# Performance work log

Hardware: AMD Instinct MI355X
Metric: run time of the kernel (lower is better)

The kernel has to match this reference:

```python
import jax, jax.numpy as jnp
import numpy as np

N_NODES = 10000
N_EDGES = 640000
D_IN = 128
D_OUT = 128


def setup_inputs() -> dict:
    key = jax.random.key(0)
    k_x, k_val, k_w, k_row, k_col = jax.random.split(key, 5)
    # Glorot init for weight, zeros for bias (matches _weight_init)
    limit = float(np.sqrt(6.0 / (D_IN + D_OUT)))
    weight = jax.random.uniform(k_w, (D_IN, D_OUT), jnp.float32, -limit, limit)
    return {
        "x": jax.random.normal(k_x, (N_NODES, D_IN), jnp.float32),
        "adj_val": jax.random.uniform(k_val, (N_EDGES,), jnp.float32),  # normalized edge weights of sparse adj
        "weight": weight,
        "bias": jnp.zeros((D_OUT,), jnp.float32),
        "adj_row": jax.random.randint(k_row, (N_EDGES,), 0, N_NODES, jnp.int32),
        "adj_col": jax.random.randint(k_col, (N_EDGES,), 0, N_NODES, jnp.int32),
    }


def reference(x, adj_val, weight, bias, adj_row, adj_col):
    # dense GEMM: h = x @ W  -> [N, D_OUT]
    h = jnp.matmul(x, weight)
    # SpMM with COO adjacency: out[r] = sum_{e: row[e]=r} val[e] * h[col[e]]
    msg = adj_val[:, None] * h[adj_col]  # [E, D_OUT] gather + scale
    out = jax.ops.segment_sum(msg, adj_row, num_segments=x.shape[0])
    return out + bias
```

## Files before the change

### kernel.cpp

```cpp
#include <hip/hip_runtime.h>

#define N_NODES 10000
#define N_EDGES 640000
#define D 128
#define NQ (N_EDGES / 4)

#define GRID1 512
#define GEMM_BLOCKS 157
#define SCAT_BLOCKS (GRID1 - GEMM_BLOCKS)
#define NBUCK 79
#define BCAP 10240
#define CAP2 128
#define QPAD2 144
#define OVF_CAP 8192
#define LSTR 136

typedef unsigned int uint32;
typedef unsigned long long u64;
typedef unsigned short u16;
using short8 = __attribute__((ext_vector_type(8))) short;
using f32x4  = __attribute__((ext_vector_type(4))) float;

__device__ __forceinline__ uint32 f2bf_bits(float f) {
    uint32 u = __float_as_uint(f);
    return (u + 0x7FFFu + ((u >> 16) & 1u)) >> 16;
}
__device__ __forceinline__ uint32 pack2(float lo, float hi) {
    return f2bf_bits(lo) | (f2bf_bits(hi) << 16);
}

__device__ __forceinline__ void ovf_push(int r, uint32 rc, int* ovf_cnt, u64* ovf) {
    int o = atomicAdd(ovf_cnt, 1);
    if (o < OVF_CAP)
        __hip_atomic_store(&ovf[o], ((u64)(uint32)r << 32) | rc,
                           __ATOMIC_RELAXED, __HIP_MEMORY_SCOPE_AGENT);
}

__global__ __launch_bounds__(256, 4) void gemm_scatter_kernel(
    const float* __restrict__ x, const float* __restrict__ w,
    const int* __restrict__ row, const int* __restrict__ col,
    const float* __restrict__ val,
    uint32* __restrict__ h2, int* __restrict__ gcnt,
    int* __restrict__ ovf_cnt, u64* __restrict__ ovf,
    uint2* __restrict__ bstore)
{
    __shared__ __align__(16) u16 Ws[128 * LSTR];
    const int t = threadIdx.x;
    const int lane = t & 63;
    const int wid  = t >> 6;

    if (blockIdx.x < GEMM_BLOCKS) {
        const int q = lane >> 4, cl = lane & 15;

        #pragma unroll
        for (int i = 0; i < 32; ++i) {
            int lin = t + i * 256;
            int c = lin & 127;
            int m = lin >> 7;
            float w0 = w[(2 * m) * D + c];
            float w1 = w[(2 * m + 1) * D + c];
            *(uint32*)&Ws[c * LSTR + 2 * m] = pack2(w0, w1);
        }

        int gr = blockIdx.x * 64 + wid * 16 + cl;
        if (gr >= N_NODES) gr = N_NODES - 1;
        const float* xrow = &x[(size_t)gr * D];
        float4 xv[8];
        #pragma unroll
        for (int kk = 0; kk < 4; ++kk) {
            xv[2 * kk]     = *(const float4*)&xrow[kk * 32 + q * 8];
            xv[2 * kk + 1] = *(const float4*)&xrow[kk * 32 + q * 8 + 4];
        }
        __syncthreads();

        f32x4 acc[8] = {};
        #pragma unroll
        for (int kk = 0; kk < 4; ++kk) {
            union { short8 s; uint32 u[4]; } af;
            float4 a = xv[2 * kk], b = xv[2 * kk + 1];
            af.u[0] = pack2(a.x, a.y); af.u[1] = pack2(a.z, a.w);
            af.u[2] = pack2(b.x, b.y); af.u[3] = pack2(b.z, b.w);
            #pragma unroll
            for (int ct = 0; ct < 8; ++ct) {
                short8 bf = *(const short8*)&Ws[(ct * 16 + cl) * LSTR + kk * 32 + q * 8];
                acc[ct] = __builtin_amdgcn_mfma_f32_16x16x32_bf16(af.s, bf, acc[ct], 0, 0, 0);
            }
        }
        #pragma unroll
        for (int reg = 0; reg < 4; ++reg) {
            int node = blockIdx.x * 64 + wid * 16 + q * 4 + reg;
            if (node < N_NODES) {
                uint32* base = h2 + (size_t)node * 64 + cl;
                #pragma unroll
                for (int ct = 0; ct < 4; ++ct)
                    base[ct * 16] = pack2(acc[ct][reg], acc[ct + 4][reg]);
            }
        }
    } else {
        int* lcnt  = (int*)Ws;
        int* lbase = (int*)Ws + 96;
        int* lcnt2 = (int*)Ws + 192;
        if (t < NBUCK) lcnt[t] = 0;
        __syncthreads();

        const int sb = blockIdx.x - GEMM_BLOCKS;
        const int4*   row4 = (const int4*)row;
        const int4*   col4 = (const int4*)col;
        const float4* val4 = (const float4*)val;

        for (int i = sb * 256 + t; i < NQ; i += SCAT_BLOCKS * 256) {
            int4 r = row4[i];
            atomicAdd(&lcnt[r.x >> 7], 1);
            atomicAdd(&lcnt[r.y >> 7], 1);
            atomicAdd(&lcnt[r.z >> 7], 1);
            atomicAdd(&lcnt[r.w >> 7], 1);
        }
        __syncthreads();
        if (t < NBUCK) {
            int c = lcnt[t];
            lbase[t] = (c > 0) ? atomicAdd(&gcnt[t], c) : 0;
            lcnt2[t] = 0;
        }
        __syncthreads();

        for (int i = sb * 256 + t; i < NQ; i += SCAT_BLOCKS * 256) {
            int4 r = row4[i]; int4 c = col4[i]; float4 v = val4[i];
            #pragma unroll
            for (int e = 0; e < 4; ++e) {
                int rr = (e == 0) ? r.x : (e == 1) ? r.y : (e == 2) ? r.z : r.w;
                int cc = (e == 0) ? c.x : (e == 1) ? c.y : (e == 2) ? c.z : c.w;
                float vv = (e == 0) ? v.x : (e == 1) ? v.y : (e == 2) ? v.z : v.w;
                uint32 rc = (uint32)cc | (f2bf_bits(vv) << 16);
                int b = rr >> 7;
                int k = atomicAdd(&lcnt2[b], 1);
                int pos = lbase[b] + k;
                if (pos < BCAP)
                    bstore[(size_t)b * BCAP + pos] = make_uint2(rc, (uint32)rr);
                else
                    ovf_push(rr, rc, ovf_cnt, ovf);
            }
        }
    }
}

__global__ __launch_bounds__(256) void spmm_kernel(
    const uint2* __restrict__ bstore, const int* __restrict__ gcnt,
    int* __restrict__ ovf_cnt, u64* __restrict__ ovf,
    const uint32* __restrict__ h2, const float* __restrict__ bias,
    float* __restrict__ out)
{
    __shared__ uint32 qbuf[4 * QPAD2];
    __shared__ int cnt[4];
    const int t = threadIdx.x;
    const int lane = t & 63;
    const int wid  = t >> 6;
    const int r0 = blockIdx.x * 4;
    const int b  = r0 >> 7;

    if (t < 4) cnt[t] = 0;
    __syncthreads();

    int n = gcnt[b]; if (n > BCAP) n = BCAP;
    for (int i = t; i < n; i += 256) {
        uint2 e = bstore[(size_t)b * BCAP + i];
        uint32 d = e.y - (uint32)r0;
        if (d < 4u) {
            int k = atomicAdd(&cnt[d], 1);
            if (k < CAP2) qbuf[d * QPAD2 + k] = e.x;
            else ovf_push((int)e.y, e.x, ovf_cnt, ovf);
        }
    }
    __syncthreads();

    const int r = r0 + wid;
    uint32* qb = &qbuf[wid * QPAD2];
    int ntot = cnt[wid]; if (ntot > CAP2) ntot = CAP2;
    if (lane < 16) qb[ntot + lane] = 0;
    __builtin_amdgcn_s_waitcnt(0);

    const int npad = (ntot + 7) & ~7;
    float a0 = 0.f, a1 = 0.f;

    uint32 rq0,rq1,rq2,rq3,rq4,rq5,rq6,rq7;
    uint32 hh0,hh1,hh2,hh3,hh4,hh5,hh6,hh7;
    rq0 = qb[0]; hh0 = h2[((rq0 & 0xFFFFu) << 6) + lane];
    rq1 = qb[1]; hh1 = h2[((rq1 & 0xFFFFu) << 6) + lane];
    rq2 = qb[2]; hh2 = h2[((rq2 & 0xFFFFu) << 6) + lane];
    rq3 = qb[3]; hh3 = h2[((rq3 & 0xFFFFu) << 6) + lane];
    rq4 = qb[4]; hh4 = h2[((rq4 & 0xFFFFu) << 6) + lane];
    rq5 = qb[5]; hh5 = h2[((rq5 & 0xFFFFu) << 6) + lane];
    rq6 = qb[6]; hh6 = h2[((rq6 & 0xFFFFu) << 6) + lane];
    rq7 = qb[7]; hh7 = h2[((rq7 & 0xFFFFu) << 6) + lane];

#define CONSUME_PREFETCH(RQ, HH, P)                                          \
    {                                                                        \
        a0 = fmaf(__uint_as_float(RQ & 0xFFFF0000u),                         \
                  __uint_as_float(HH << 16), a0);                            \
        a1 = fmaf(__uint_as_float(RQ & 0xFFFF0000u),                         \
                  __uint_as_float(HH & 0xFFFF0000u), a1);                    \
        uint32 rn = qb[j + 8 + P];                                           \
        RQ = rn; HH = h2[((rn & 0xFFFFu) << 6) + lane];                      \
    }

    for (int j = 0; j < npad; j += 8) {
        CONSUME_PREFETCH(rq0, hh0, 0)
        CONSUME_PREFETCH(rq1, hh1, 1)
        CONSUME_PREFETCH(rq2, hh2, 2)
        CONSUME_PREFETCH(rq3, hh3, 3)
        CONSUME_PREFETCH(rq4, hh4, 4)
        CONSUME_PREFETCH(rq5, hh5, 5)
        CONSUME_PREFETCH(rq6, hh6, 6)
        CONSUME_PREFETCH(rq7, hh7, 7)
    }
#undef CONSUME_PREFETCH

    int novf = __hip_atomic_load(ovf_cnt, __ATOMIC_RELAXED, __HIP_MEMORY_SCOPE_AGENT);
    if (novf > OVF_CAP) novf = OVF_CAP;
    for (int k = 0; k < novf; ++k) {
        u64 e = __hip_atomic_load(&ovf[k], __ATOMIC_RELAXED, __HIP_MEMORY_SCOPE_AGENT);
        if ((uint32)(e >> 32) == (uint32)r) {
            uint32 qq = (uint32)e;
            uint32 hv = h2[((qq & 0xFFFFu) << 6) + lane];
            a0 = fmaf(__uint_as_float(qq & 0xFFFF0000u), __uint_as_float(hv << 16), a0);
            a1 = fmaf(__uint_as_float(qq & 0xFFFF0000u), __uint_as_float(hv & 0xFFFF0000u), a1);
        }
    }

    out[(size_t)r * D + lane]      = a0 + bias[lane];
    out[(size_t)r * D + 64 + lane] = a1 + bias[lane + 64];
}

extern "C" void kernel_launch(void* const* d_in, const int* in_sizes, int n_in,
                              void* d_out, int out_size, void* d_ws, size_t ws_size,
                              hipStream_t stream)
{
    const float* x    = (const float*)d_in[0];
    const float* aval = (const float*)d_in[1];
    const float* w    = (const float*)d_in[2];
    const float* bias = (const float*)d_in[3];
    const int* arow   = (const int*)d_in[4];
    const int* acol   = (const int*)d_in[5];

    char* ws = (char*)d_ws;
    uint32* h2     = (uint32*)(ws);
    int*    gcnt   = (int*)(ws + 2560000);
    int*    ovfcnt = (int*)(ws + 2560320);
    u64*    ovf    = (u64*)(ws + 2560384);
    uint2*  bstore = (uint2*)(ws + 2625920);

    hipMemsetAsync(ws + 2560000, 0, 324, stream);

    gemm_scatter_kernel<<<GRID1, 256, 0, stream>>>(
        x, w, arow, acol, aval, h2, gcnt, ovfcnt, ovf, bstore);
    spmm_kernel<<<N_NODES / 4, 256, 0, stream>>>(
        bstore, gcnt, ovfcnt, ovf, h2, bias, (float*)d_out);
}
```

Before: 121.7 us.

## Replace global-atomic bucket scatter with per-chunk fixed slots and drop memset

The edge scatter now gives each of 256 chunk blocks a fixed slot region per row bucket, using only LDS atomics and a single pass, so it no longer needs a count pass or global atomics. Overflow goes to per-chunk spill arrays, and the memset launch is removed because every count is written unconditionally. The SpMM kernel handles 8 rows per block and scans all 256×96 slots of a bucket, which are padded and mostly empty. The W load is also vectorized to float4. The cost is that the consumer reads more sparsely populated slots and every thread checks the spill counts.

```diff
diff --git a/kernel.cpp b/kernel.cpp
--- a/kernel.cpp
+++ b/kernel.cpp
@@ -5,18 +5,19 @@
 #define D 128
 #define NQ (N_EDGES / 4)
 
-#define GRID1 512
+#define NCHUNK 256
+#define QPC (NQ / NCHUNK)
 #define GEMM_BLOCKS 157
-#define SCAT_BLOCKS (GRID1 - GEMM_BLOCKS)
+#define GRID1 (NCHUNK + GEMM_BLOCKS)
 #define NBUCK 79
-#define BCAP 10240
+#define CCAP 96
+#define SLOTS (NCHUNK * CCAP)
+#define SPILLCAP 2500
 #define CAP2 128
 #define QPAD2 144
-#define OVF_CAP 8192
 #define LSTR 136
 
 typedef unsigned int uint32;
-typedef unsigned long long u64;
 typedef unsigned short u16;
 using short8 = __attribute__((ext_vector_type(8))) short;
 using f32x4  = __attribute__((ext_vector_type(4))) float;
@@ -27,42 +28,76 @@
 }
 __device__ __forceinline__ uint32 pack2(float lo, float hi) {
     return f2bf_bits(lo) | (f2bf_bits(hi) << 16);
-}
-
-__device__ __forceinline__ void ovf_push(int r, uint32 rc, int* ovf_cnt, u64* ovf) {
-    int o = atomicAdd(ovf_cnt, 1);
-    if (o < OVF_CAP)
-        __hip_atomic_store(&ovf[o], ((u64)(uint32)r << 32) | rc,
-                           __ATOMIC_RELAXED, __HIP_MEMORY_SCOPE_AGENT);
 }
 
 __global__ __launch_bounds__(256, 4) void gemm_scatter_kernel(
     const float* __restrict__ x, const float* __restrict__ w,
     const int* __restrict__ row, const int* __restrict__ col,
     const float* __restrict__ val,
-    uint32* __restrict__ h2, int* __restrict__ gcnt,
-    int* __restrict__ ovf_cnt, u64* __restrict__ ovf,
-    uint2* __restrict__ bstore)
+    uint32* __restrict__ h2, int* __restrict__ cnts,
+    int* __restrict__ spillcnt, uint2* __restrict__ bstore,
+    uint2* __restrict__ spill)
 {
     __shared__ __align__(16) u16 Ws[128 * LSTR];
     const int t = threadIdx.x;
-    const int lane = t & 63;
-    const int wid  = t >> 6;
-
-    if (blockIdx.x < GEMM_BLOCKS) {
+
+    if (blockIdx.x < NCHUNK) {
+        int* lcnt = (int*)Ws;
+        if (t < 96) lcnt[t] = 0;
+        __syncthreads();
+
+        const int sb = blockIdx.x;
+        const int4*   row4 = (const int4*)row;
+        const int4*   col4 = (const int4*)col;
+        const float4* val4 = (const float4*)val;
+        const int i0 = sb * QPC;
+        for (int i = i0 + t; i < i0 + QPC; i += 256) {
+            int4 r = row4[i]; int4 c = col4[i]; float4 v = val4[i];
+            #pragma unroll
+            for (int e = 0; e < 4; ++e) {
+                int rr = (e == 0) ? r.x : (e == 1) ? r.y : (e == 2) ? r.z : r.w;
+                int cc = (e == 0) ? c.x : (e == 1) ? c.y : (e == 2) ? c.z : c.w;
+                float vv = (e == 0) ? v.x : (e == 1) ? v.y : (e == 2) ? v.z : v.w;
+                uint32 rc = (uint32)cc | (f2bf_bits(vv) << 16);
+                int b = rr >> 7;
+                int k = atomicAdd(&lcnt[b], 1);
+                if (k < CCAP)
+                    bstore[(size_t)(b * NCHUNK + sb) * CCAP + k] =
+                        make_uint2(rc, (uint32)rr);
+                else {
+                    int ks = atomicAdd(&lcnt[95], 1);
+                    spill[(size_t)sb * SPILLCAP + ks] = make_uint2(rc, (uint32)rr);
+                }
+            }
+        }
+        __syncthreads();
+        if (t < NBUCK) {
+            int c = lcnt[t];
+            cnts[t * NCHUNK + sb] = (c < CCAP) ? c : CCAP;
+        }
+        if (t == 96) spillcnt[sb] = lcnt[95];
+    } else {
+        const int g = blockIdx.x - NCHUNK;
+        const int lane = t & 63;
+        const int wid  = t >> 6;
         const int q = lane >> 4, cl = lane & 15;
 
-        #pragma unroll
-        for (int i = 0; i < 32; ++i) {
+        const float4* w4 = (const float4*)w;
+        #pragma unroll
+        for (int i = 0; i < 8; ++i) {
             int lin = t + i * 256;
-            int c = lin & 127;
-            int m = lin >> 7;
-            float w0 = w[(2 * m) * D + c];
-            float w1 = w[(2 * m + 1) * D + c];
-            *(uint32*)&Ws[c * LSTR + 2 * m] = pack2(w0, w1);
-        }
-
-        int gr = blockIdx.x * 64 + wid * 16 + cl;
+            int m  = lin >> 5;
+            int qc = lin & 31;
+            float4 r0 = w4[(2 * m) * 32 + qc];
+            float4 r1 = w4[(2 * m + 1) * 32 + qc];
+            int c = qc * 4;
+            *(uint32*)&Ws[(c + 0) * LSTR + 2 * m] = pack2(r0.x, r1.x);
+            *(uint32*)&Ws[(c + 1) * LSTR + 2 * m] = pack2(r0.y, r1.y);
+            *(uint32*)&Ws[(c + 2) * LSTR + 2 * m] = pack2(r0.z, r1.z);
+            *(uint32*)&Ws[(c + 3) * LSTR + 2 * m] = pack2(r0.w, r1.w);
+        }
+
+        int gr = g * 64 + wid * 16 + cl;
         if (gr >= N_NODES) gr = N_NODES - 1;
         const float* xrow = &x[(size_t)gr * D];
         float4 xv[8];
@@ -88,7 +123,7 @@
         }
         #pragma unroll
         for (int reg = 0; reg < 4; ++reg) {
-            int node = blockIdx.x * 64 + wid * 16 + q * 4 + reg;
+            int node = g * 64 + wid * 16 + q * 4 + reg;
             if (node < N_NODES) {
                 uint32* base = h2 + (size_t)node * 64 + cl;
                 #pragma unroll
@@ -96,101 +131,75 @@
                     base[ct * 16] = pack2(acc[ct][reg], acc[ct + 4][reg]);
             }
         }
-    } else {
-        int* lcnt  = (int*)Ws;
-        int* lbase = (int*)Ws + 96;
-        int* lcnt2 = (int*)Ws + 192;
-        if (t < NBUCK) lcnt[t] = 0;
-        __syncthreads();
-
-        const int sb = blockIdx.x - GEMM_BLOCKS;
-        const int4*   row4 = (const int4*)row;
-        const int4*   col4 = (const int4*)col;
-        const float4* val4 = (const float4*)val;
-
-        for (int i = sb * 256 + t; i < NQ; i += SCAT_BLOCKS * 256) {
-            int4 r = row4[i];
-            atomicAdd(&lcnt[r.x >> 7], 1);
-            atomicAdd(&lcnt[r.y >> 7], 1);
-            atomicAdd(&lcnt[r.z >> 7], 1);
-            atomicAdd(&lcnt[r.w >> 7], 1);
-        }
-        __syncthreads();
-        if (t < NBUCK) {
-            int c = lcnt[t];
-            lbase[t] = (c > 0) ? atomicAdd(&gcnt[t], c) : 0;
-            lcnt2[t] = 0;
-        }
-        __syncthreads();
-
-        for (int i = sb * 256 + t; i < NQ; i += SCAT_BLOCKS * 256) {
-            int4 r = row4[i]; int4 c = col4[i]; float4 v = val4[i];
-            #pragma unroll
-            for (int e = 0; e < 4; ++e) {
-                int rr = (e == 0) ? r.x : (e == 1) ? r.y : (e == 2) ? r.z : r.w;
-                int cc = (e == 0) ? c.x : (e == 1) ? c.y : (e == 2) ? c.z : c.w;
-                float vv = (e == 0) ? v.x : (e == 1) ? v.y : (e == 2) ? v.z : v.w;
-                uint32 rc = (uint32)cc | (f2bf_bits(vv) << 16);
-                int b = rr >> 7;
-                int k = atomicAdd(&lcnt2[b], 1);
-                int pos = lbase[b] + k;
-                if (pos < BCAP)
-                    bstore[(size_t)b * BCAP + pos] = make_uint2(rc, (uint32)rr);
-                else
-                    ovf_push(rr, rc, ovf_cnt, ovf);
-            }
-        }
     }
 }
 
 __global__ __launch_bounds__(256) void spmm_kernel(
-    const uint2* __restrict__ bstore, const int* __restrict__ gcnt,
-    int* __restrict__ ovf_cnt, u64* __restrict__ ovf,
+    const uint2* __restrict__ bstore, const int* __restrict__ cnts,
+    const int* __restrict__ spillcnt, const uint2* __restrict__ spill,
     const uint32* __restrict__ h2, const float* __restrict__ bias,
     float* __restrict__ out)
 {
-    __shared__ uint32 qbuf[4 * QPAD2];
-    __shared__ int cnt[4];
+    __shared__ uint32 qbuf[8 * QPAD2];
+    __shared__ int lcnts[NCHUNK];
+    __shared__ int cnt[8];
     const int t = threadIdx.x;
     const int lane = t & 63;
     const int wid  = t >> 6;
-    const int r0 = blockIdx.x * 4;
+    const int r0 = blockIdx.x * 8;
     const int b  = r0 >> 7;
 
-    if (t < 4) cnt[t] = 0;
+    lcnts[t] = cnts[b * NCHUNK + t];
+    if (t < 8) cnt[t] = 0;
     __syncthreads();
 
-    int n = gcnt[b]; if (n > BCAP) n = BCAP;
-    for (int i = t; i < n; i += 256) {
-        uint2 e = bstore[(size_t)b * BCAP + i];
-        uint32 d = e.y - (uint32)r0;
-        if (d < 4u) {
-            int k = atomicAdd(&cnt[d], 1);
-            if (k < CAP2) qbuf[d * QPAD2 + k] = e.x;
-            else ovf_push((int)e.y, e.x, ovf_cnt, ovf);
+    for (int i = t; i < SLOTS; i += 256) {
+        int ch = i / CCAP;
+        int sl = i - ch * CCAP;
+        if (sl < lcnts[ch]) {
+            uint2 e = bstore[(size_t)b * SLOTS + i];
+            uint32 d = e.y - (uint32)r0;
+            if (d < 8u) {
+                int k = atomicAdd(&cnt[d], 1);
+                if (k < CAP2) qbuf[d * QPAD2 + k] = e.x;
+            }
+        }
+    }
+    {
+        int sc = spillcnt[t];
+        for (int k = 0; k < sc; ++k) {
+            uint2 e = spill[(size_t)t * SPILLCAP + k];
+            uint32 d = e.y - (uint32)r0;
+            if (d < 8u) {
+                int k2 = atomicAdd(&cnt[d], 1);
+                if (k2 < CAP2) qbuf[d * QPAD2 + k2] = e.x;
+            }
         }
     }
     __syncthreads();
 
-    const int r = r0 + wid;
-    uint32* qb = &qbuf[wid * QPAD2];
-    int ntot = cnt[wid]; if (ntot > CAP2) ntot = CAP2;
-    if (lane < 16) qb[ntot + lane] = 0;
-    __builtin_amdgcn_s_waitcnt(0);
-
-    const int npad = (ntot + 7) & ~7;
-    float a0 = 0.f, a1 = 0.f;
-
-    uint32 rq0,rq1,rq2,rq3,rq4,rq5,rq6,rq7;
-    uint32 hh0,hh1,hh2,hh3,hh4,hh5,hh6,hh7;
-    rq0 = qb[0]; hh0 = h2[((rq0 & 0xFFFFu) << 6) + lane];
-    rq1 = qb[1]; hh1 = h2[((rq1 & 0xFFFFu) << 6) + lane];
-    rq2 = qb[2]; hh2 = h2[((rq2 & 0xFFFFu) << 6) + lane];
-    rq3 = qb[3]; hh3 = h2[((rq3 & 0xFFFFu) << 6) + lane];
-    rq4 = qb[4]; hh4 = h2[((rq4 & 0xFFFFu) << 6) + lane];
-    rq5 = qb[5]; hh5 = h2[((rq5 & 0xFFFFu) << 6) + lane];
-    rq6 = qb[6]; hh6 = h2[((rq6 & 0xFFFFu) << 6) + lane];
-    rq7 = qb[7]; hh7 = h2[((rq7 & 0xFFFFu) << 6) + lane];
+    for (int half = 0; half < 2; ++half) {
+        const int d = wid * 2 + half;
+        const int r = r0 + d;
+        uint32* qb = &qbuf[d * QPAD2];
+        const int ntot = cnt[d];
+        float a0 = 0.f, a1 = 0.f;
+
+        if (ntot <= CAP2) {
+            if (lane < 16) qb[ntot + lane] = 0;
+            __builtin_amdgcn_s_waitcnt(0);
+
+            const int npad = (ntot + 7) & ~7;
+            uint32 rq0,rq1,rq2,rq3,rq4,rq5,rq6,rq7;
+            uint32 hh0,hh1,hh2,hh3,hh4,hh5,hh6,hh7;
+            rq0 = qb[0]; hh0 = h2[((rq0 & 0xFFFFu) << 6) + lane];
+            rq1 = qb[1]; hh1 = h2[((rq1 & 0xFFFFu) << 6) + lane];
+            rq2 = qb[2]; hh2 = h2[((rq2 & 0xFFFFu) << 6) + lane];
+            rq3 = qb[3]; hh3 = h2[((rq3 & 0xFFFFu) << 6) + lane];
+            rq4 = qb[4]; hh4 = h2[((rq4 & 0xFFFFu) << 6) + lane];
+            rq5 = qb[5]; hh5 = h2[((rq5 & 0xFFFFu) << 6) + lane];
+            rq6 = qb[6]; hh6 = h2[((rq6 & 0xFFFFu) << 6) + lane];
+            rq7 = qb[7]; hh7 = h2[((rq7 & 0xFFFFu) << 6) + lane];
 
 #define CONSUME_PREFETCH(RQ, HH, P)                                          \
     {                                                                        \
@@ -202,32 +211,49 @@
         RQ = rn; HH = h2[((rn & 0xFFFFu) << 6) + lane];                      \
     }
 
-    for (int j = 0; j < npad; j += 8) {
-        CONSUME_PREFETCH(rq0, hh0, 0)
-        CONSUME_PREFETCH(rq1, hh1, 1)
-        CONSUME_PREFETCH(rq2, hh2, 2)
-        CONSUME_PREFETCH(rq3, hh3, 3)
-        CONSUME_PREFETCH(rq4, hh4, 4)
-        CONSUME_PREFETCH(rq5, hh5, 5)
-        CONSUME_PREFETCH(rq6, hh6, 6)
-        CONSUME_PREFETCH(rq7, hh7, 7)
-    }
+            for (int j = 0; j < npad; j += 8) {
+                CONSUME_PREFETCH(rq0, hh0, 0)
+                CONSUME_PREFETCH(rq1, hh1, 1)
+                CONSUME_PREFETCH(rq2, hh2, 2)
+                CONSUME_PREFETCH(rq3, hh3, 3)
+                CONSUME_PREFETCH(rq4, hh4, 4)
+                CONSUME_PREFETCH(rq5, hh5, 5)
+                CONSUME_PREFETCH(rq6, hh6, 6)
+                CONSUME_PREFETCH(rq7, hh7, 7)
+            }
 #undef CONSUME_PREFETCH
-
-    int novf = __hip_atomic_load(ovf_cnt, __ATOMIC_RELAXED, __HIP_MEMORY_SCOPE_AGENT);
-    if (novf > OVF_CAP) novf = OVF_CAP;
-    for (int k = 0; k < novf; ++k) {
-        u64 e = __hip_atomic_load(&ovf[k], __ATOMIC_RELAXED, __HIP_MEMORY_SCOPE_AGENT);
-        if ((uint32)(e >> 32) == (uint32)r) {
-            uint32 qq = (uint32)e;
-            uint32 hv = h2[((qq & 0xFFFFu) << 6) + lane];
-            a0 = fmaf(__uint_as_float(qq & 0xFFFF0000u), __uint_as_float(hv << 16), a0);
-            a1 = fmaf(__uint_as_float(qq & 0xFFFF0000u), __uint_as_float(hv & 0xFFFF0000u), a1);
-        }
-    }
-
-    out[(size_t)r * D + lane]      = a0 + bias[lane];
-    out[(size_t)r * D + 64 + lane] = a1 + bias[lane + 64];
+        } else {
+            for (int i = 0; i < SLOTS; ++i) {
+                int ch = i / CCAP, sl = i - ch * CCAP;
+                if (sl < lcnts[ch]) {
+                    uint2 e = bstore[(size_t)b * SLOTS + i];
+                    if (e.y == (uint32)r) {
+                        uint32 hv = h2[((e.x & 0xFFFFu) << 6) + lane];
+                        a0 = fmaf(__uint_as_float(e.x & 0xFFFF0000u),
+                                  __uint_as_float(hv << 16), a0);
+                        a1 = fmaf(__uint_as_float(e.x & 0xFFFF0000u),
+                                  __uint_as_float(hv & 0xFFFF0000u), a1);
+                    }
+                }
+            }
+            for (int ch = 0; ch < NCHUNK; ++ch) {
+                int sc = spillcnt[ch];
+                for (int k = 0; k < sc; ++k) {
+                    uint2 e = spill[(size_t)ch * SPILLCAP + k];
+                    if (e.y == (uint32)r) {
+                        uint32 hv = h2[((e.x & 0xFFFFu) << 6) + lane];
+                        a0 = fmaf(__uint_as_float(e.x & 0xFFFF0000u),
+                                  __uint_as_float(hv << 16), a0);
+                        a1 = fmaf(__uint_as_float(e.x & 0xFFFF0000u),
+                                  __uint_as_float(hv & 0xFFFF0000u), a1);
+                    }
+                }
+            }
+        }
+
+        out[(size_t)r * D + lane]      = a0 + bias[lane];
+        out[(size_t)r * D + 64 + lane] = a1 + bias[lane + 64];
+    }
 }
 
 extern "C" void kernel_launch(void* const* d_in, const int* in_sizes, int n_in,
@@ -242,16 +268,15 @@
     const int* acol   = (const int*)d_in[5];
 
     char* ws = (char*)d_ws;
-    uint32* h2     = (uint32*)(ws);
-    int*    gcnt   = (int*)(ws + 2560000);
-    int*    ovfcnt = (int*)(ws + 2560320);
-    u64*    ovf    = (u64*)(ws + 2560384);
-    uint2*  bstore = (uint2*)(ws + 2625920);
-
-    hipMemsetAsync(ws + 2560000, 0, 324, stream);
+    uint32* h2       = (uint32*)(ws);
+    int*    cnts     = (int*)(ws + 2560000);
+    int*    spillcnt = (int*)(ws + 2640896);
+    uint2*  bstore   = (uint2*)(ws + 2641920);
+    uint2*  spill    = (uint2*)(ws + 18173952);
+
 
     gemm_scatter_kernel<<<GRID1, 256, 0, stream>>>(
-        x, w, arow, acol, aval, h2, gcnt, ovfcnt, ovf, bstore);
-    spmm_kernel<<<N_NODES / 4, 256, 0, stream>>>(
-        bstore, gcnt, ovfcnt, ovf, h2, bias, (float*)d_out);
-}
+        x, w, arow, acol, aval, h2, cnts, spillcnt, bstore, spill);
+    spmm_kernel<<<N_NODES / 8, 256, 0, stream>>>(
+        bstore, cnts, spillcnt, spill, h2, bias, (float*)d_out);
+}
```

Measured after the change: 123.4 us. About the same (+1.4%).
